# Optimization experiments

Hardware: AMD Instinct MI355X
Metric: run time of the kernel (lower is better)

## Reference

```python
import jax, jax.numpy as jnp
import numpy as np

B, S, D = 2, 4096, 768
H, DH = 12, 64
BLK = 64
NB = S // BLK
L, F = 2, 3072
V, POS = 50358, 4096
NS, NL = 8, 2
NKV = 8  # 3 sliding-window + 2 global + 3 random key blocks per query block
SCALE = 1.0 / np.sqrt(DH)


def layer_norm(x, g, b):
    m = jnp.mean(x, -1, keepdims=True)
    v = jnp.mean(jnp.square(x - m), -1, keepdims=True)
    return (x - m) * jax.lax.rsqrt(v + 1e-12) * g + b


def block_sparse_attention(x, mask, w_qkv, b_qkv, rand_blocks):
    # x: [B,S,D], w_qkv: [3,D,D], rand_blocks: [NB,3] int block ids
    qkv = jnp.einsum('bsd,tde->tbse', x, w_qkv) + b_qkv[:, None, None, :]
    q, k, v = [a.reshape(B, S, H, DH).transpose(0, 2, 1, 3) for a in qkv]  # [B,H,S,DH]
    qb = q.reshape(B, H, NB, BLK, DH)
    kb = k.reshape(B, H, NB, BLK, DH)
    vb = v.reshape(B, H, NB, BLK, DH)
    ar = jnp.arange(NB)
    win = jnp.clip(ar[:, None] + jnp.arange(-1, 2)[None, :], 0, NB - 1)  # [NB,3]
    glb = jnp.broadcast_to(jnp.array([0, NB - 1]), (NB, 2))              # [NB,2]
    idx = jnp.concatenate([win, glb, rand_blocks], axis=1)               # [NB,NKV]
    kg = kb[:, :, idx].reshape(B, H, NB, NKV * BLK, DH)                  # gathered keys
    vg = vb[:, :, idx].reshape(B, H, NB, NKV * BLK, DH)
    mg = mask.reshape(B, NB, BLK)[:, idx].reshape(B, NB, NKV * BLK)
    scores = jnp.einsum('bhnqd,bhnkd->bhnqk', qb, kg) * SCALE
    scores = scores + (mg[:, None, :, None, :] - 1.0) * 1e9
    out = jnp.einsum('bhnqk,bhnkd->bhnqd', jax.nn.softmax(scores, -1), vg)  # [B,H,NB,BLK,DH]
    # global query blocks (first/last) attend densely to the full sequence
    qg = jnp.concatenate([qb[:, :, 0], qb[:, :, NB - 1]], axis=2)  # [B,H,2*BLK,DH]
    sg = jnp.einsum('bhqd,bhkd->bhqk', qg, k) * SCALE + (mask[:, None, None, :] - 1.0) * 1e9
    og = jnp.einsum('bhqk,bhkd->bhqd', jax.nn.softmax(sg, -1), v)
    out = out.at[:, :, 0].set(og[:, :, :BLK]).at[:, :, NB - 1].set(og[:, :, BLK:])
    return out.reshape(B, H, S, DH).transpose(0, 2, 1, 3).reshape(B, S, D)


def setup_inputs() -> dict:
    key = jax.random.key(0)
    ks = iter(jax.random.split(key, 40))
    p = lambda shape: (0.02 * jax.random.normal(next(ks), shape)).astype(jnp.float32)
    inp = {}
    inp['input_ids'] = jax.random.randint(next(ks), (B, S), 0, V, dtype=jnp.int32)
    inp['attention_mask'] = jnp.ones((B, S), jnp.float32)
    inp['token_type_ids'] = jnp.zeros((B, S), jnp.int32)
    st = jax.random.randint(next(ks), (B, NS), 0, S - 65, dtype=jnp.int32)
    ln_ = jax.random.randint(next(ks), (B, NS), 1, 65, dtype=jnp.int32)
    inp['spans'] = jnp.stack([st, st + ln_], axis=-1)  # [B,NS,2], start < end
    inp['rand_blocks'] = jax.random.randint(next(ks), (NB, 3), 0, NB, dtype=jnp.int32)
    inp['word_emb'] = p((V, D))
    inp['pos_emb'] = p((POS, D))
    inp['type_emb'] = p((2, D))
    inp['emb_ln_g'] = jnp.ones((D,), jnp.float32)
    inp['emb_ln_b'] = jnp.zeros((D,), jnp.float32)
    inp['qkv_w'] = p((L, 3, D, D))
    inp['qkv_b'] = jnp.zeros((L, 3, D), jnp.float32)
    inp['attn_out_w'] = p((L, D, D))
    inp['attn_out_b'] = jnp.zeros((L, D), jnp.float32)
    inp['ln1_g'] = jnp.ones((L, D), jnp.float32)
    inp['ln1_b'] = jnp.zeros((L, D), jnp.float32)
    inp['ff1_w'] = p((L, D, F))
    inp['ff1_b'] = jnp.zeros((L, F), jnp.float32)
    inp['ff2_w'] = p((L, F, D))
    inp['ff2_b'] = jnp.zeros((L, D), jnp.float32)
    inp['ln2_g'] = jnp.ones((L, D), jnp.float32)
    inp['ln2_b'] = jnp.zeros((L, D), jnp.float32)
    inp['head_w'] = p((D, NL))
    inp['head_b'] = jnp.zeros((NL,), jnp.float32)
    return inp


def reference(input_ids, attention_mask, token_type_ids, spans, rand_blocks,
              word_emb, pos_emb, type_emb, emb_ln_g, emb_ln_b,
              qkv_w, qkv_b, attn_out_w, attn_out_b, ln1_g, ln1_b,
              ff1_w, ff1_b, ff2_w, ff2_b, ln2_g, ln2_b, head_w, head_b):
    h = word_emb[input_ids] + pos_emb[None, :S] + type_emb[token_type_ids]
    h = layer_norm(h, emb_ln_g, emb_ln_b)
    for l in range(L):
        a = block_sparse_attention(h, attention_mask, qkv_w[l], qkv_b[l], rand_blocks)
        h = layer_norm(h + a @ attn_out_w[l] + attn_out_b[l], ln1_g[l], ln1_b[l])
        ff = jax.nn.gelu(h @ ff1_w[l] + ff1_b[l]) @ ff2_w[l] + ff2_b[l]
        h = layer_norm(h + ff, ln2_g[l], ln2_b[l])
    # span mean pooling: mean of h[b, s:e] for each (s,e) span
    starts, ends = spans[..., 0], spans[..., 1]
    pos = jnp.arange(S)
    span_mask = ((pos >= starts[..., None]) & (pos < ends[..., None])).astype(h.dtype)  # [B,NS,S]
    ent = jnp.einsum('bns,bsd->bnd', span_mask, h) / (ends - starts)[..., None].astype(h.dtype)
    pred = ent @ head_w + head_b  # [B,NS,NL]
    return pred.reshape(B * NS, NL)
```

## Files before the change

kernel.cpp:

```cpp
#include <hip/hip_runtime.h>

constexpr int B = 2, S = 4096, D = 768, H = 12, DH = 64, BLK = 64, NB = 64, NKV = 8;
constexpr int F = 3072, NS = 8, M = B * S;
constexpr int NCH = 4;
constexpr float SCALE = 0.125f;
constexpr float L2E = 1.44269504088896f;
constexpr long HD = (long)M * D;

using u16 = unsigned short;
using u32 = unsigned int;
using bf16 = __bf16;
using bf16x8 = __attribute__((ext_vector_type(8))) bf16;
using f32x4 = __attribute__((ext_vector_type(4))) float;

constexpr long DD = (long)D * D;
constexpr long DF = (long)D * F;
constexpr long OFF_AO  = 6 * DD;
constexpr long OFF_FF1 = 8 * DD;
constexpr long OFF_FF2 = 8 * DD + 2 * DF;

__device__ __forceinline__ u16 f2bf(float x) {
  u32 u = __builtin_bit_cast(u32, x);
  u = (u + 0x7fffu + ((u >> 16) & 1u)) >> 16;
  return (u16)u;
}
__device__ __forceinline__ u32 pack2(float a, float b) {
  return (u32)f2bf(a) | ((u32)f2bf(b) << 16);
}
__device__ __forceinline__ float fast_gelu(float x) {
  float u = 0.7978845608028654f * (x + 0.044715f * x * x * x);
  float t = __expf(u + u);
  return x - x * __builtin_amdgcn_rcpf(t + 1.f);
}

__device__ __forceinline__ void gload16(const void* g, void* l) {
  __builtin_amdgcn_global_load_lds(
      (const __attribute__((address_space(1))) u32*)g,
      (__attribute__((address_space(3))) u32*)l, 16, 0, 0);
}

__global__ __launch_bounds__(256) void wtrans_kern(
    const float* __restrict__ in, u16* __restrict__ out, int K, int N, long inz, long outz)
{
  in += (long)blockIdx.z * inz; out += (long)blockIdx.z * outz;
  __shared__ float T[32][33];
  const int n0 = blockIdx.x * 32, k0 = blockIdx.y * 32;
  const int c = threadIdx.x & 31, r8 = threadIdx.x >> 5;
  #pragma unroll
  for (int i = 0; i < 4; ++i)
    T[r8 + i * 8][c] = in[(long)(k0 + r8 + i * 8) * N + n0 + c];
  __syncthreads();
  #pragma unroll
  for (int i = 0; i < 4; ++i)
    out[(long)(n0 + r8 + i * 8) * K + k0 + c] = f2bf(T[c][r8 + i * 8]);
}

__global__ __launch_bounds__(256) void embed_ln_kern(
    const int* __restrict__ ids, const int* __restrict__ tt,
    const float* __restrict__ we, const float* __restrict__ pe, const float* __restrict__ te,
    const float* __restrict__ g, const float* __restrict__ bb,
    float* __restrict__ h, u16* __restrict__ hb)
{
  __shared__ float sa[4], sb[4];
  const long i = blockIdx.x;
  const int tid = threadIdx.x;
  const int s = (int)(i & (S - 1));
  const long wo = (long)ids[i] * D;
  const long to = (long)tt[i] * D;
  const long po = (long)s * D;
  float x0 = we[wo + tid]       + pe[po + tid]       + te[to + tid];
  float x1 = we[wo + tid + 256] + pe[po + tid + 256] + te[to + tid + 256];
  float x2 = we[wo + tid + 512] + pe[po + tid + 512] + te[to + tid + 512];
  float sm = x0 + x1 + x2, sq = x0*x0 + x1*x1 + x2*x2;
  #pragma unroll
  for (int o = 32; o; o >>= 1) { sm += __shfl_xor(sm, o); sq += __shfl_xor(sq, o); }
  if ((tid & 63) == 0) { sa[tid >> 6] = sm; sb[tid >> 6] = sq; }
  __syncthreads();
  sm = sa[0] + sa[1] + sa[2] + sa[3];
  sq = sb[0] + sb[1] + sb[2] + sb[3];
  const float mean = sm * (1.f / D);
  const float var  = sq * (1.f / D) - mean * mean;
  const float rs   = rsqrtf(var + 1e-12f);
  float* row = h + i * D;
  u16* rb = hb + i * D;
  float y0 = (x0 - mean) * rs * g[tid]       + bb[tid];
  float y1 = (x1 - mean) * rs * g[tid + 256] + bb[tid + 256];
  float y2 = (x2 - mean) * rs * g[tid + 512] + bb[tid + 512];
  row[tid] = y0; row[tid + 256] = y1; row[tid + 512] = y2;
  rb[tid] = f2bf(y0); rb[tid + 256] = f2bf(y1); rb[tid + 512] = f2bf(y2);
}

__global__ __launch_bounds__(256) void ln_kern(
    float* __restrict__ h, const float* __restrict__ g, const float* __restrict__ bb,
    u16* __restrict__ hb)
{
  const long i = (long)blockIdx.x * 4 + (threadIdx.x >> 6);
  const int lane = threadIdx.x & 63;
  const int c = lane * 4;
  float* row = h + i * D;
  u16* rb = hb + i * D;
  float4 x0 = *(const float4*)(row + c);
  float4 x1 = *(const float4*)(row + c + 256);
  float4 x2 = *(const float4*)(row + c + 512);
  float sm = x0.x+x0.y+x0.z+x0.w + x1.x+x1.y+x1.z+x1.w + x2.x+x2.y+x2.z+x2.w;
  float sq = x0.x*x0.x+x0.y*x0.y+x0.z*x0.z+x0.w*x0.w
           + x1.x*x1.x+x1.y*x1.y+x1.z*x1.z+x1.w*x1.w
           + x2.x*x2.x+x2.y*x2.y+x2.z*x2.z+x2.w*x2.w;
  #pragma unroll
  for (int o = 32; o; o >>= 1) { sm += __shfl_xor(sm, o); sq += __shfl_xor(sq, o); }
  const float mean = sm * (1.f / D);
  const float var  = sq * (1.f / D) - mean * mean;
  const float rs   = rsqrtf(var + 1e-12f);
  float4 g0 = *(const float4*)(g + c),  g1 = *(const float4*)(g + c + 256),
         g2 = *(const float4*)(g + c + 512);
  float4 b0 = *(const float4*)(bb + c), b1 = *(const float4*)(bb + c + 256),
         b2 = *(const float4*)(bb + c + 512);
  float4 y0 = make_float4((x0.x-mean)*rs*g0.x+b0.x, (x0.y-mean)*rs*g0.y+b0.y,
                          (x0.z-mean)*rs*g0.z+b0.z, (x0.w-mean)*rs*g0.w+b0.w);
  float4 y1 = make_float4((x1.x-mean)*rs*g1.x+b1.x, (x1.y-mean)*rs*g1.y+b1.y,
                          (x1.z-mean)*rs*g1.z+b1.z, (x1.w-mean)*rs*g1.w+b1.w);
  float4 y2 = make_float4((x2.x-mean)*rs*g2.x+b2.x, (x2.y-mean)*rs*g2.y+b2.y,
                          (x2.z-mean)*rs*g2.z+b2.z, (x2.w-mean)*rs*g2.w+b2.w);
  *(float4*)(row + c)       = y0;
  *(float4*)(row + c + 256) = y1;
  *(float4*)(row + c + 512) = y2;
  *(uint2*)(rb + c)       = make_uint2(pack2(y0.x, y0.y), pack2(y0.z, y0.w));
  *(uint2*)(rb + c + 256) = make_uint2(pack2(y1.x, y1.y), pack2(y1.z, y1.w));
  *(uint2*)(rb + c + 512) = make_uint2(pack2(y2.x, y2.y), pack2(y2.z, y2.w));
}

__global__ __launch_bounds__(256) void mgemm_kern(
    const u16* __restrict__ A, const u16* __restrict__ Wt,
    const float* __restrict__ bias, void* __restrict__ Cv,
    int N, int K, long wz, long bz, long cz, int mode, int ksplit)
{
  const int z = blockIdx.z;
  int k0 = 0, kend = K;
  if (ksplit > 1) {
    const int kch = K / ksplit;
    k0 = z * kch; kend = k0 + kch;
  } else {
    Wt += (long)z * wz; bias += (long)z * bz;
  }
  const int gx = gridDim.x;
  const int nwg = gx * gridDim.y;
  int bid = blockIdx.y * gx + blockIdx.x;
  bid = (bid & 7) * (nwg >> 3) + (bid >> 3);
  const long bm = (long)(bid / gx) * 128;
  const int bn = (bid % gx) * 128;

  const int tid = threadIdx.x;
  const int lane = tid & 63, w = tid >> 6;
  const int wm = w >> 1, wn = w & 1;
  const int ls = lane >> 4, lr = lane & 15;

  __shared__ u16 LB[32768];
  u16* const St0 = LB;
  u16* const St1 = LB + 16384;

  f32x4 acc[4][4];
  #pragma unroll
  for (int i = 0; i < 4; ++i)
    #pragma unroll
    for (int j = 0; j < 4; ++j)
      acc[i][j] = (f32x4){0.f, 0.f, 0.f, 0.f};

  auto STAGE = [&](u16* buf, int kk) {
    #pragma unroll
    for (int c = 0; c < 4; ++c) {
      const int n = (w * 4 + c) * 64 + lane;
      const int row = n >> 3;
      const int kc2 = (n & 7) ^ (row & 7);
      gload16(A  + (bm + row) * K + kk + kc2 * 8, buf + (w * 4 + c) * 512);
      gload16(Wt + (long)(bn + row) * K + kk + kc2 * 8, buf + 8192 + (w * 4 + c) * 512);
    }
  };

  STAGE(St0, k0);
  int cur = 0;
  for (int kk = k0; kk < kend; kk += 64) {
    if (kk + 64 < kend) {
      STAGE(cur ? St0 : St1, kk + 64);
      asm volatile("s_waitcnt vmcnt(8)" ::: "memory");
    } else {
      asm volatile("s_waitcnt vmcnt(0)" ::: "memory");
    }
    __builtin_amdgcn_s_barrier();
    __builtin_amdgcn_sched_barrier(0);
    const u16* AsL = cur ? St1 : St0;
    const u16* BsL = AsL + 8192;
    __builtin_amdgcn_s_setprio(1);
    #pragma unroll
    for (int ks = 0; ks < 2; ++ks) {
      bf16x8 af[4], bv[4];
      const int kc = ks * 4 + ls;
      const int sw = (kc ^ (lr & 7)) << 3;
      #pragma unroll
      for (int mf = 0; mf < 4; ++mf)
        af[mf] = *(const bf16x8*)&AsL[(wm * 64 + mf * 16 + lr) * 64 + sw];
      #pragma unroll
      for (int nf = 0; nf < 4; ++nf)
        bv[nf] = *(const bf16x8*)&BsL[(wn * 64 + nf * 16 + lr) * 64 + sw];
      #pragma unroll
      for (int mf = 0; mf < 4; ++mf)
        #pragma unroll
        for (int nf = 0; nf < 4; ++nf)
          acc[mf][nf] = __builtin_amdgcn_mfma_f32_16x16x32_bf16(
              af[mf], bv[nf], acc[mf][nf], 0, 0, 0);
    }
    __builtin_amdgcn_s_setprio(0);
    __builtin_amdgcn_s_barrier();
    cur ^= 1;
  }

  float* Cf = (float*)Cv + (long)z * cz;
  u16*   Cu = (u16*)Cv  + (long)z * cz;
  const int r0 = ls * 4;
  const bool addb = (ksplit == 1) || (z == 0);

  if (mode == 1 || (mode == 4 && bn < 1536)) {
    const int t = (mode == 4) ? (bn / 768) : 0;
    const int cl0 = (mode == 4) ? (bn - t * 768) : bn;
    const int Nt = (mode == 4) ? 768 : N;
    u16* Cd = (mode == 4) ? (Cu + (long)t * HD) : Cu;
    #pragma unroll
    for (int nf = 0; nf < 4; ++nf) {
      const int col = wn * 64 + nf * 16 + lr;
      const float bvv = bias[bn + col];
      #pragma unroll
      for (int mf = 0; mf < 4; ++mf) {
        #pragma unroll
        for (int r = 0; r < 4; ++r) {
          const int rowl = wm * 64 + mf * 16 + r0 + r;
          float vv = acc[mf][nf][r] + bvv;
          if (mode == 1) vv = fast_gelu(vv);
          LB[rowl * 128 + (col ^ ((rowl & 7) << 3))] = f2bf(vv);
        }
      }
    }
    __syncthreads();
    const int c0 = (tid & 15) * 8;
    #pragma unroll
    for (int i = 0; i < 8; ++i) {
      const int gr = (tid >> 4) + i * 16;
      uint4 v4 = *(const uint4*)&LB[gr * 128 + (c0 ^ ((gr & 7) << 3))];
      *(uint4*)(Cd + (bm + gr) * Nt + cl0 + c0) = v4;
    }
    return;
  }

  if (mode == 4) {
    #pragma unroll
    for (int nf = 0; nf < 4; ++nf) {
      const int cl = bn - 1536 + wn * 64 + nf * 16 + lr;
      const int hcol = cl >> 6, dcol = cl & 63;
      const float bvv = bias[1536 + cl];
      #pragma unroll
      for (int mf = 0; mf < 4; ++mf) {
        const long t0 = bm + wm * 64 + mf * 16 + r0;
        const int bb2 = (int)(t0 >> 12), s0 = (int)(t0 & (S - 1));
        const float v0 = acc[mf][nf][0] + bvv, v1 = acc[mf][nf][1] + bvv;
        const float v2 = acc[mf][nf][2] + bvv, v3 = acc[mf][nf][3] + bvv;
        *(uint2*)(Cu + 2 * HD + (((long)bb2 * H + hcol) * 64 + dcol) * S + s0) =
            make_uint2(pack2(v0, v1), pack2(v2, v3));
      }
    }
    return;
  }

  #pragma unroll
  for (int nf = 0; nf < 4; ++nf) {
    const int col = bn + wn * 64 + nf * 16 + lr;
    const float bvv = addb ? bias[col] : 0.f;
    #pragma unroll
    for (int mf = 0; mf < 4; ++mf) {
      #pragma unroll
      for (int r = 0; r < 4; ++r) {
        const long row = bm + wm * 64 + mf * 16 + r0 + r;
        float vv = acc[mf][nf][r] + bvv;
        if (mode == 2) {
          if (ksplit > 1) atomicAdd(&Cf[row * N + col], vv);
          else            Cf[row * N + col] += vv;
        } else {
          Cf[row * N + col] = vv;
        }
      }
    }
  }
}

__global__ __launch_bounds__(256) void mattn_kern(
    const u16* __restrict__ q, const u16* __restrict__ k, const u16* __restrict__ vt,
    const float* __restrict__ mask, const int* __restrict__ rb,
    u16* __restrict__ ctx, float* __restrict__ part)
{
  int lin = blockIdx.x;
  lin = (lin & 7) * 210 + (lin >> 3);
  const int x  = lin % 70;
  const int hh = (lin / 70) % H;
  const int b  = lin / 840;

  int qb, kv0, nkv, qb2 = 0, ch = 0, dense;
  if (x < 62) { dense = 0; qb = x + 1; kv0 = 0; nkv = NKV; }
  else {
    dense = 1;
    const int dx = x - 62;
    qb2 = dx >> 2; ch = dx & 3;
    qb = qb2 ? NB - 1 : 0; kv0 = ch * (NB / NCH); nkv = NB / NCH;
  }
  const int tid = threadIdx.x, lane = tid & 63, w = tid >> 6;
  const int lr = lane & 15, hi = lane >> 4;

  __shared__ u16 KV[2][8192];
  __shared__ u16 Ps[64][72];

  const long qrow0 = (long)b * S + qb * 64;
  bf16x8 qf[2];
  {
    const u16* qp = q + (qrow0 + w * 16 + lr) * D + hh * 64 + hi * 8;
    qf[0] = *(const bf16x8*)(qp);
    qf[1] = *(const bf16x8*)(qp + 32);
  }
  const long vtbase = (((long)b * H + hh) * 64) * S;

  bf16x8 ones8;
  #pragma unroll
  for (int i = 0; i < 8; ++i) ones8[i] = __builtin_bit_cast(bf16, (u16)0x3F80);

  auto kbof = [&](int j) -> int {
    if (dense) return kv0 + j;
    if (j < 3) return qb - 1 + j;
    if (j == 3) return 0;
    if (j == 4) return NB - 1;
    return rb[qb * 3 + (j - 5)];
  };

  auto STAGE = [&](u16* st, int kb) {
    const long krow0 = (long)b * S + kb * 64;
    #pragma unroll
    for (int c = 0; c < 2; ++c) {
      const int n = (w * 2 + c) * 64 + lane;
      const int row = n >> 3;
      const int g2 = (n & 7) ^ (row & 7);
      gload16(k + (krow0 + row) * D + hh * 64 + g2 * 8, st + (w * 2 + c) * 512);
      gload16(vt + vtbase + (long)row * S + kb * 64 + g2 * 8, st + 4096 + (w * 2 + c) * 512);
    }
  };

  f32x4 acc[4];
  #pragma unroll
  for (int nf = 0; nf < 4; ++nf) acc[nf] = (f32x4){0.f, 0.f, 0.f, 0.f};
  f32x4 lacc = (f32x4){0.f, 0.f, 0.f, 0.f};
  float m_run = -1e30f;

  const float C2 = SCALE * L2E;

  STAGE(KV[0], kbof(0));

  for (int jj = 0; jj < nkv; ++jj) {
    if (jj + 1 < nkv) {
      STAGE(KV[(jj + 1) & 1], kbof(jj + 1));
      asm volatile("s_waitcnt vmcnt(4)" ::: "memory");
    } else {
      asm volatile("s_waitcnt vmcnt(0)" ::: "memory");
    }
    __builtin_amdgcn_s_barrier();
    __builtin_amdgcn_sched_barrier(0);

    const u16* Ks = KV[jj & 1];
    const u16* Vs = Ks + 4096;
    const long kmrow = (long)b * S + kbof(jj) * 64;

    f32x4 sc[4];
    #pragma unroll
    for (int kf = 0; kf < 4; ++kf) sc[kf] = (f32x4){0.f, 0.f, 0.f, 0.f};
    __builtin_amdgcn_s_setprio(1);
    #pragma unroll
    for (int kc = 0; kc < 2; ++kc) {
      #pragma unroll
      for (int kf = 0; kf < 4; ++kf) {
        const int g2 = ((kc * 4 + hi) ^ (lr & 7)) << 3;
        bf16x8 kfr = *(const bf16x8*)&Ks[(kf * 16 + lr) * 64 + g2];
        sc[kf] = __builtin_amdgcn_mfma_f32_16x16x32_bf16(kfr, qf[kc], sc[kf], 0, 0, 0);
      }
    }
    __builtin_amdgcn_s_setprio(0);

    float sv[4][4];
    float mx = -3.0e38f;
    #pragma unroll
    for (int kf = 0; kf < 4; ++kf) {
      float4 mk4 = *(const float4*)(mask + kmrow + kf * 16 + hi * 4);
      const float mka[4] = {mk4.x, mk4.y, mk4.z, mk4.w};
      #pragma unroll
      for (int r = 0; r < 4; ++r) {
        sv[kf][r] = sc[kf][r] * C2 + (mka[r] - 1.f) * (1e9f * L2E);
        mx = fmaxf(mx, sv[kf][r]);
      }
    }
    mx = fmaxf(mx, __shfl_xor(mx, 16));
    mx = fmaxf(mx, __shfl_xor(mx, 32));
    const bool need = mx > m_run + 8.f;
    if (__any((int)need)) {
      const float mn = fmaxf(m_run, mx);
      const float al = exp2f(m_run - mn);
      m_run = mn;
      #pragma unroll
      for (int r = 0; r < 4; ++r) {
        const float alr = __shfl(al, (lane & 48) | (hi * 4 + r));
        lacc[r] *= alr;
        acc[0][r] *= alr; acc[1][r] *= alr; acc[2][r] *= alr; acc[3][r] *= alr;
      }
    }
    {
      const int prow = w * 16 + lr;
      #pragma unroll
      for (int kf = 0; kf < 4; ++kf) {
        u32 lo = pack2(exp2f(sv[kf][0] - m_run), exp2f(sv[kf][1] - m_run));
        u32 hi2 = pack2(exp2f(sv[kf][2] - m_run), exp2f(sv[kf][3] - m_run));
        *(uint2*)&Ps[prow][kf * 16 + hi * 4] = make_uint2(lo, hi2);
      }
    }

    __builtin_amdgcn_s_setprio(1);
    #pragma unroll
    for (int kc = 0; kc < 2; ++kc) {
      bf16x8 pf = *(const bf16x8*)&Ps[w * 16 + lr][kc * 32 + hi * 8];
      #pragma unroll
      for (int nf = 0; nf < 4; ++nf) {
        const int g2 = ((kc * 4 + hi) ^ (lr & 7)) << 3;
        bf16x8 vfr = *(const bf16x8*)&Vs[(nf * 16 + lr) * 64 + g2];
        acc[nf] = __builtin_amdgcn_mfma_f32_16x16x32_bf16(pf, vfr, acc[nf], 0, 0, 0);
      }
      lacc = __builtin_amdgcn_mfma_f32_16x16x32_bf16(pf, ones8, lacc, 0, 0, 0);
    }
    __builtin_amdgcn_s_setprio(0);

    __builtin_amdgcn_s_barrier();
  }

  if (!dense) {
    #pragma unroll
    for (int r = 0; r < 4; ++r) {
      const float inv = 1.f / lacc[r];
      const int prow = w * 16 + hi * 4 + r;
      Ps[prow][ 0 + lr] = f2bf(acc[0][r] * inv);
      Ps[prow][16 + lr] = f2bf(acc[1][r] * inv);
      Ps[prow][32 + lr] = f2bf(acc[2][r] * inv);
      Ps[prow][48 + lr] = f2bf(acc[3][r] * inv);
    }
    __syncthreads();
    const int r2 = tid >> 2, c2 = (tid & 3) * 16;
    uint4 v0 = *(const uint4*)&Ps[r2][c2];
    uint4 v1 = *(const uint4*)&Ps[r2][c2 + 8];
    u16* op = ctx + (qrow0 + r2) * D + hh * 64 + c2;
    *(uint4*)(op)     = v0;
    *(uint4*)(op + 8) = v1;
  } else {
    const long pb = ((((long)b * H + hh) * 2 + qb2) * NCH + ch) * (64 * 68);
    #pragma unroll
    for (int r = 0; r < 4; ++r) {
      const float m_r = __shfl(m_run, (lane & 48) | (hi * 4 + r));
      float* pp = part + pb + (w * 16 + hi * 4 + r) * 68;
      pp[ 0 + lr] = acc[0][r];
      pp[16 + lr] = acc[1][r];
      pp[32 + lr] = acc[2][r];
      pp[48 + lr] = acc[3][r];
      if (lr == 0) { pp[64] = m_r; pp[65] = lacc[r]; }
    }
  }
}

__global__ __launch_bounds__(256) void attn_combine_kern(
    const float* __restrict__ part, u16* __restrict__ ctx)
{
  const int g = blockIdx.x;
  const int qb2 = g & 1;
  const int hh = (g >> 1) % H;
  const int b  = g / (2 * H);
  const int r  = threadIdx.x >> 2;
  const int d0 = (threadIdx.x & 3) * 16;
  const long pb = (long)g * NCH * 64 * 68;
  float mg = -1e30f;
  for (int ch = 0; ch < NCH; ++ch)
    mg = fmaxf(mg, part[pb + ch * 64 * 68 + r * 68 + 64]);
  float lg = 0.f;
  float a[16] = {};
  for (int ch = 0; ch < NCH; ++ch) {
    const float* pp = part + pb + ch * 64 * 68 + r * 68;
    const float w = exp2f(pp[64] - mg);
    lg += pp[65] * w;
    #pragma unroll
    for (int i = 0; i < 4; ++i) {
      float4 t4 = *(const float4*)(pp + d0 + i * 4);
      a[i*4+0] += t4.x * w; a[i*4+1] += t4.y * w; a[i*4+2] += t4.z * w; a[i*4+3] += t4.w * w;
    }
  }
  const int qb = qb2 ? NB - 1 : 0;
  const float inv = 1.f / lg;
  u16* op = ctx + ((long)b * S + qb * 64 + r) * D + hh * 64 + d0;
  #pragma unroll
  for (int i = 0; i < 4; ++i)
    *(uint2*)(op + i * 4) = make_uint2(pack2(a[i*4+0]*inv, a[i*4+1]*inv),
                                       pack2(a[i*4+2]*inv, a[i*4+3]*inv));
}

__global__ __launch_bounds__(256) void span_head_kern(
    const float* __restrict__ h, const int* __restrict__ spans,
    const float* __restrict__ hw, const float* __restrict__ hb, float* __restrict__ out)
{
  __shared__ float s0[4], s1[4];
  const int bn = blockIdx.x;
  const int tid = threadIdx.x;
  const int st = spans[bn * 2], en = spans[bn * 2 + 1];
  const int b = bn >> 3;
  float a0 = 0.f, a1 = 0.f, a2 = 0.f;
  for (int s = st; s < en; ++s) {
    const float* row = h + ((long)b * S + s) * D;
    a0 += row[tid]; a1 += row[tid + 256]; a2 += row[tid + 512];
  }
  const float inv = 1.f / (float)(en - st);
  a0 *= inv; a1 *= inv; a2 *= inv;
  float p0 = a0 * hw[tid * 2]     + a1 * hw[(tid + 256) * 2]     + a2 * hw[(tid + 512) * 2];
  float p1 = a0 * hw[tid * 2 + 1] + a1 * hw[(tid + 256) * 2 + 1] + a2 * hw[(tid + 512) * 2 + 1];
  #pragma unroll
  for (int o = 32; o; o >>= 1) { p0 += __shfl_xor(p0, o); p1 += __shfl_xor(p1, o); }
  if ((tid & 63) == 0) { s0[tid >> 6] = p0; s1[tid >> 6] = p1; }
  __syncthreads();
  if (tid == 0) {
    out[bn * 2]     = s0[0] + s0[1] + s0[2] + s0[3] + hb[0];
    out[bn * 2 + 1] = s1[0] + s1[1] + s1[2] + s1[3] + hb[1];
  }
}

extern "C" void kernel_launch(void* const* d_in, const int* in_sizes, int n_in,
                              void* d_out, int out_size, void* d_ws, size_t ws_size,
                              hipStream_t stream) {
  const int*   input_ids  = (const int*)  d_in[0];
  const float* attn_mask  = (const float*)d_in[1];
  const int*   tok_type   = (const int*)  d_in[2];
  const int*   spans      = (const int*)  d_in[3];
  const int*   rand_blk   = (const int*)  d_in[4];
  const float* word_emb   = (const float*)d_in[5];
  const float* pos_emb    = (const float*)d_in[6];
  const float* type_emb   = (const float*)d_in[7];
  const float* emb_g      = (const float*)d_in[8];
  const float* emb_b      = (const float*)d_in[9];
  const float* qkv_w      = (const float*)d_in[10];
  const float* qkv_b      = (const float*)d_in[11];
  const float* aow        = (const float*)d_in[12];
  const float* aob        = (const float*)d_in[13];
  const float* ln1g       = (const float*)d_in[14];
  const float* ln1b       = (const float*)d_in[15];
  const float* ff1w       = (const float*)d_in[16];
  const float* ff1b       = (const float*)d_in[17];
  const float* ff2w       = (const float*)d_in[18];
  const float* ff2b       = (const float*)d_in[19];
  const float* ln2g       = (const float*)d_in[20];
  const float* ln2b       = (const float*)d_in[21];
  const float* headw      = (const float*)d_in[22];
  const float* headb      = (const float*)d_in[23];

  float* ws    = (float*)d_ws;
  float* h     = ws;
  u16*   qkvb  = (u16*)(ws + HD);
  u16*   ffb   = (u16*)(ws + HD);
  u16*   ctx16 = (u16*)(ws + 3 * HD);
  u16*   hb    = (u16*)(ws + 3 * HD + HD/2);
  float* part  = ws + 4 * HD;
  u16*   wb    = (u16*)(ws + 4 * HD + HD/4);

  wtrans_kern<<<dim3(24, 24, 6), dim3(256), 0, stream>>>(qkv_w, wb, D, D, DD, DD);
  wtrans_kern<<<dim3(24, 24, 2), dim3(256), 0, stream>>>(aow, wb + OFF_AO, D, D, DD, DD);
  wtrans_kern<<<dim3(96, 24, 2), dim3(256), 0, stream>>>(ff1w, wb + OFF_FF1, D, F, DF, DF);
  wtrans_kern<<<dim3(24, 96, 2), dim3(256), 0, stream>>>(ff2w, wb + OFF_FF2, F, D, DF, DF);

  embed_ln_kern<<<dim3(M), dim3(256), 0, stream>>>(
      input_ids, tok_type, word_emb, pos_emb, type_emb, emb_g, emb_b, h, hb);

  for (int l = 0; l < 2; ++l) {
    mgemm_kern<<<dim3(18, 64, 1), dim3(256), 0, stream>>>(
        hb, wb + (long)l * 3 * DD, qkv_b + (long)l * 3 * D, qkvb, 2304, D, 0, 0, 0, 4, 1);
    mattn_kern<<<dim3(1680), dim3(256), 0, stream>>>(
        qkvb, qkvb + HD, qkvb + 2 * HD, attn_mask, rand_blk, ctx16, part);
    attn_combine_kern<<<dim3(B * H * 2), dim3(256), 0, stream>>>(part, ctx16);
    mgemm_kern<<<dim3(6, 64, 2), dim3(256), 0, stream>>>(
        ctx16, wb + OFF_AO + (long)l * DD, aob + (long)l * D, h, D, D, 0, 0, 0, 2, 2);
    ln_kern<<<dim3(M / 4), dim3(256), 0, stream>>>(h, ln1g + (long)l * D, ln1b + (long)l * D, hb);
    mgemm_kern<<<dim3(24, 64, 1), dim3(256), 0, stream>>>(
        hb, wb + OFF_FF1 + (long)l * DF, ff1b + (long)l * F, ffb, F, D, 0, 0, 0, 1, 1);
    mgemm_kern<<<dim3(6, 64, 2), dim3(256), 0, stream>>>(
        ffb, wb + OFF_FF2 + (long)l * DF, ff2b + (long)l * D, h, D, F, 0, 0, 0, 2, 2);
    ln_kern<<<dim3(M / 4), dim3(256), 0, stream>>>(h, ln2g + (long)l * D, ln2b + (long)l * D, hb);
  }

  span_head_kern<<<dim3(B * NS), dim3(256), 0, stream>>>(h, spans, headw, headb, (float*)d_out);
}
```

Baseline: 679.6 us.

## Vectorize embedding LN, prefetch attention mask, drop split-K for out-proj

Rewrites the embedding+layernorm kernel so each wavefront handles one row with float4 loads and packed bf16 stores, which removes the shared-memory reduction and the block barrier. In the sparse attention kernel the key mask for the next block is loaded into registers during the current iteration, so it is no longer a dependent global load on the critical path. The attention output-projection GEMM also drops from a split-K of 2 to 1. That removes partial-sum accumulation but leaves fewer workgroups for the K=768 GEMM.

```diff
diff --git a/kernel.cpp b/kernel.cpp
--- a/kernel.cpp
+++ b/kernel.cpp
@@ -61,33 +61,52 @@
     const float* __restrict__ g, const float* __restrict__ bb,
     float* __restrict__ h, u16* __restrict__ hb)
 {
-  __shared__ float sa[4], sb[4];
-  const long i = blockIdx.x;
-  const int tid = threadIdx.x;
+  const long i = (long)blockIdx.x * 4 + (threadIdx.x >> 6);
+  const int lane = threadIdx.x & 63;
+  const int c = lane * 4;
   const int s = (int)(i & (S - 1));
   const long wo = (long)ids[i] * D;
   const long to = (long)tt[i] * D;
   const long po = (long)s * D;
-  float x0 = we[wo + tid]       + pe[po + tid]       + te[to + tid];
-  float x1 = we[wo + tid + 256] + pe[po + tid + 256] + te[to + tid + 256];
-  float x2 = we[wo + tid + 512] + pe[po + tid + 512] + te[to + tid + 512];
-  float sm = x0 + x1 + x2, sq = x0*x0 + x1*x1 + x2*x2;
+  float4 x0, x1, x2;
+  {
+    float4 a0 = *(const float4*)(we + wo + c),       p0 = *(const float4*)(pe + po + c),
+           t0 = *(const float4*)(te + to + c);
+    float4 a1 = *(const float4*)(we + wo + c + 256), p1 = *(const float4*)(pe + po + c + 256),
+           t1 = *(const float4*)(te + to + c + 256);
+    float4 a2 = *(const float4*)(we + wo + c + 512), p2 = *(const float4*)(pe + po + c + 512),
+           t2 = *(const float4*)(te + to + c + 512);
+    x0 = make_float4(a0.x+p0.x+t0.x, a0.y+p0.y+t0.y, a0.z+p0.z+t0.z, a0.w+p0.w+t0.w);
+    x1 = make_float4(a1.x+p1.x+t1.x, a1.y+p1.y+t1.y, a1.z+p1.z+t1.z, a1.w+p1.w+t1.w);
+    x2 = make_float4(a2.x+p2.x+t2.x, a2.y+p2.y+t2.y, a2.z+p2.z+t2.z, a2.w+p2.w+t2.w);
+  }
+  float sm = x0.x+x0.y+x0.z+x0.w + x1.x+x1.y+x1.z+x1.w + x2.x+x2.y+x2.z+x2.w;
+  float sq = x0.x*x0.x+x0.y*x0.y+x0.z*x0.z+x0.w*x0.w
+           + x1.x*x1.x+x1.y*x1.y+x1.z*x1.z+x1.w*x1.w
+           + x2.x*x2.x+x2.y*x2.y+x2.z*x2.z+x2.w*x2.w;
   #pragma unroll
   for (int o = 32; o; o >>= 1) { sm += __shfl_xor(sm, o); sq += __shfl_xor(sq, o); }
-  if ((tid & 63) == 0) { sa[tid >> 6] = sm; sb[tid >> 6] = sq; }
-  __syncthreads();
-  sm = sa[0] + sa[1] + sa[2] + sa[3];
-  sq = sb[0] + sb[1] + sb[2] + sb[3];
   const float mean = sm * (1.f / D);
   const float var  = sq * (1.f / D) - mean * mean;
   const float rs   = rsqrtf(var + 1e-12f);
+  float4 g0 = *(const float4*)(g + c),  g1 = *(const float4*)(g + c + 256),
+         g2 = *(const float4*)(g + c + 512);
+  float4 b0 = *(const float4*)(bb + c), b1 = *(const float4*)(bb + c + 256),
+         b2 = *(const float4*)(bb + c + 512);
   float* row = h + i * D;
   u16* rb = hb + i * D;
-  float y0 = (x0 - mean) * rs * g[tid]       + bb[tid];
-  float y1 = (x1 - mean) * rs * g[tid + 256] + bb[tid + 256];
-  float y2 = (x2 - mean) * rs * g[tid + 512] + bb[tid + 512];
-  row[tid] = y0; row[tid + 256] = y1; row[tid + 512] = y2;
-  rb[tid] = f2bf(y0); rb[tid + 256] = f2bf(y1); rb[tid + 512] = f2bf(y2);
+  float4 y0 = make_float4((x0.x-mean)*rs*g0.x+b0.x, (x0.y-mean)*rs*g0.y+b0.y,
+                          (x0.z-mean)*rs*g0.z+b0.z, (x0.w-mean)*rs*g0.w+b0.w);
+  float4 y1 = make_float4((x1.x-mean)*rs*g1.x+b1.x, (x1.y-mean)*rs*g1.y+b1.y,
+                          (x1.z-mean)*rs*g1.z+b1.z, (x1.w-mean)*rs*g1.w+b1.w);
+  float4 y2 = make_float4((x2.x-mean)*rs*g2.x+b2.x, (x2.y-mean)*rs*g2.y+b2.y,
+                          (x2.z-mean)*rs*g2.z+b2.z, (x2.w-mean)*rs*g2.w+b2.w);
+  *(float4*)(row + c)       = y0;
+  *(float4*)(row + c + 256) = y1;
+  *(float4*)(row + c + 512) = y2;
+  *(uint2*)(rb + c)       = make_uint2(pack2(y0.x, y0.y), pack2(y0.z, y0.w));
+  *(uint2*)(rb + c + 256) = make_uint2(pack2(y1.x, y1.y), pack2(y1.z, y1.w));
+  *(uint2*)(rb + c + 512) = make_uint2(pack2(y2.x, y2.y), pack2(y2.z, y2.w));
 }
 
 __global__ __launch_bounds__(256) void ln_kern(
@@ -355,7 +374,16 @@
 
   const float C2 = SCALE * L2E;
 
+  float4 mk4[4];
+  auto LOADMASK = [&](int kb) {
+    const long r = (long)b * S + kb * 64;
+    #pragma unroll
+    for (int kf = 0; kf < 4; ++kf)
+      mk4[kf] = *(const float4*)(mask + r + kf * 16 + hi * 4);
+  };
+
   STAGE(KV[0], kbof(0));
+  LOADMASK(kbof(0));
 
   for (int jj = 0; jj < nkv; ++jj) {
     if (jj + 1 < nkv) {
@@ -369,7 +397,6 @@
 
     const u16* Ks = KV[jj & 1];
     const u16* Vs = Ks + 4096;
-    const long kmrow = (long)b * S + kbof(jj) * 64;
 
     f32x4 sc[4];
     #pragma unroll
@@ -390,8 +417,7 @@
     float mx = -3.0e38f;
     #pragma unroll
     for (int kf = 0; kf < 4; ++kf) {
-      float4 mk4 = *(const float4*)(mask + kmrow + kf * 16 + hi * 4);
-      const float mka[4] = {mk4.x, mk4.y, mk4.z, mk4.w};
+      const float mka[4] = {mk4[kf].x, mk4[kf].y, mk4[kf].z, mk4[kf].w};
       #pragma unroll
       for (int r = 0; r < 4; ++r) {
         sv[kf][r] = sc[kf][r] * C2 + (mka[r] - 1.f) * (1e9f * L2E);
@@ -435,6 +461,8 @@
       lacc = __builtin_amdgcn_mfma_f32_16x16x32_bf16(pf, ones8, lacc, 0, 0, 0);
     }
     __builtin_amdgcn_s_setprio(0);
+
+    if (jj + 1 < nkv) LOADMASK(kbof(jj + 1));
 
     __builtin_amdgcn_s_barrier();
   }
@@ -575,7 +603,7 @@
   wtrans_kern<<<dim3(96, 24, 2), dim3(256), 0, stream>>>(ff1w, wb + OFF_FF1, D, F, DF, DF);
   wtrans_kern<<<dim3(24, 96, 2), dim3(256), 0, stream>>>(ff2w, wb + OFF_FF2, F, D, DF, DF);
 
-  embed_ln_kern<<<dim3(M), dim3(256), 0, stream>>>(
+  embed_ln_kern<<<dim3(M / 4), dim3(256), 0, stream>>>(
       input_ids, tok_type, word_emb, pos_emb, type_emb, emb_g, emb_b, h, hb);
 
   for (int l = 0; l < 2; ++l) {
@@ -584,8 +612,8 @@
     mattn_kern<<<dim3(1680), dim3(256), 0, stream>>>(
         qkvb, qkvb + HD, qkvb + 2 * HD, attn_mask, rand_blk, ctx16, part);
     attn_combine_kern<<<dim3(B * H * 2), dim3(256), 0, stream>>>(part, ctx16);
-    mgemm_kern<<<dim3(6, 64, 2), dim3(256), 0, stream>>>(
-        ctx16, wb + OFF_AO + (long)l * DD, aob + (long)l * D, h, D, D, 0, 0, 0, 2, 2);
+    mgemm_kern<<<dim3(6, 64, 1), dim3(256), 0, stream>>>(
+        ctx16, wb + OFF_AO + (long)l * DD, aob + (long)l * D, h, D, D, 0, 0, 0, 2, 1);
     ln_kern<<<dim3(M / 4), dim3(256), 0, stream>>>(h, ln1g + (long)l * D, ln1b + (long)l * D, hb);
     mgemm_kern<<<dim3(24, 64, 1), dim3(256), 0, stream>>>(
         hb, wb + OFF_FF1 + (long)l * DF, ff1b + (long)l * F, ffb, F, D, 0, 0, 0, 1, 1);
```

Measured after the change: 651.1 us, median of 2. 1.04x faster.
